# Kernel tuning notes

Hardware: AMD Instinct MI355X
Metric: run time of the kernel (lower is better)

Reference implementation:

```python
import jax, jax.numpy as jnp
import numpy as np

NUM_NODES = 113      # nodes (ROIs) per graph, from __init__ default
NUM_GRAPHS = 4096    # graphs in the batch
IN_DIM, HID, EMB = 3, 128, 1024
GROUPS = 8
EPS = 1e-5


def _kaiming(key, fan_in, fan_out_dim, shape):
    # kaiming_normal_(mode='fan_out', nonlinearity='leaky_relu') with default a=sqrt(5)->gain irrelevant here;
    # torch uses gain = sqrt(2/(1+0.01^2)) for leaky_relu default slope; simple faithful-scale normal init.
    gain = jnp.sqrt(2.0 / (1.0 + 0.01 ** 2)).astype(jnp.float32)
    std = gain / jnp.sqrt(jnp.float32(fan_out_dim))
    return jax.random.normal(key, shape, dtype=jnp.float32) * std


def setup_inputs() -> dict:
    key = jax.random.key(0)
    ks = jax.random.split(key, 8)
    N = NUM_GRAPHS * NUM_NODES
    x = jax.random.normal(ks[0], (N, IN_DIM), dtype=jnp.float32)
    batch = jnp.repeat(jnp.arange(NUM_GRAPHS, dtype=jnp.int32), NUM_NODES)
    return {
        "x": x,
        "roi_scaler": jnp.ones((NUM_NODES, IN_DIM), dtype=jnp.float32),
        "W1": _kaiming(ks[1], IN_DIM, HID, (IN_DIM, HID)),
        "b1": jnp.zeros((HID,), jnp.float32),
        "gn_g": jnp.ones((HID,), jnp.float32),
        "gn_b": jnp.zeros((HID,), jnp.float32),
        "W2": _kaiming(ks[2], HID, HID, (HID, HID)),
        "b2": jnp.zeros((HID,), jnp.float32),
        "W3": _kaiming(ks[3], HID, 512, (HID, 512)),
        "b3": jnp.zeros((512,), jnp.float32),
        "bn_g": jnp.ones((512,), jnp.float32),
        "bn_b": jnp.zeros((512,), jnp.float32),
        "W4": _kaiming(ks[4], 512, EMB, (512, EMB)),
        "b4": jnp.zeros((EMB,), jnp.float32),
        "batch": batch,
    }


def _group_norm(h, gamma, beta):
    # torch GroupNorm on [N, C]: per-row, per-group normalization
    N, C = h.shape
    hg = h.reshape(N, GROUPS, C // GROUPS)
    mu = hg.mean(axis=-1, keepdims=True)
    var = hg.var(axis=-1, keepdims=True)
    hn = ((hg - mu) * jax.lax.rsqrt(var + EPS)).reshape(N, C)
    return hn * gamma + beta


def reference(x, roi_scaler, W1, b1, gn_g, gn_b, W2, b2, W3, b3, bn_g, bn_b, W4, b4, batch):
    # per-ROI learned scaling, tiled across graphs (node order is graph-major)
    h = x * jnp.tile(roi_scaler, (NUM_GRAPHS, 1))            # [N, 3]
    # node_net: Linear -> GroupNorm(8) -> LeakyReLU(0.2) -> Linear
    h = h @ W1 + b1                                          # [N, 128]
    h = _group_norm(h, gn_g, gn_b)
    h = jnp.where(h > 0, h, 0.2 * h)
    h = h @ W2 + b2                                          # [N, 128]
    # global_max_pool: segment max over graph id
    z = jax.ops.segment_max(h, batch, num_segments=NUM_GRAPHS)  # [G, 128]
    # projection: Linear -> BatchNorm1d (batch stats, no running stats) -> ReLU -> Linear
    p = z @ W3 + b3                                          # [G, 512]
    mu = p.mean(axis=0)
    var = p.var(axis=0)
    p = (p - mu) * jax.lax.rsqrt(var + EPS) * bn_g + bn_b
    p = jax.nn.relu(p)
    out = p @ W4 + b4                                        # [G, 1024]
    # F.normalize(p=2, dim=1)
    nrm = jnp.sqrt(jnp.sum(out * out, axis=1, keepdims=True))
    return out / jnp.maximum(nrm, 1e-12)
```

## Files before the change

kernel.cpp:

```cpp
#include <hip/hip_runtime.h>
#include <hip/hip_bf16.h>

typedef _Float16 f16_8 __attribute__((ext_vector_type(8)));
typedef _Float16 f16_4 __attribute__((ext_vector_type(4)));
typedef float f32x4 __attribute__((ext_vector_type(4)));

#define NNODES 113
#define NGRAPH 4096

#define Z_OFF    0u
#define PH_OFF   2097152u
#define PSUM_OFF 6291456u
#define PSQ_OFF  6815744u
#define PSN_OFF  7340032u
#define GC_OFF   10485760u
#define SA_OFF   10489856u
#define SD_OFF   10491904u
#define W2P_OFF  10493952u
#define W4P_OFF  10559488u

__global__ __launch_bounds__(256) void k0_prep(
    const float* __restrict__ W2, const float* __restrict__ W4,
    const float* __restrict__ W1, const float* __restrict__ b1,
    _Float16* __restrict__ w2p, _Float16* __restrict__ w4p,
    float* __restrict__ gc) {
  int b = blockIdx.x, t = threadIdx.x;
  if (b < 256) {
    __shared__ _Float16 T[32 * 72];
    int kt = b >> 4, nc = b & 15;
    int row = t >> 3, c8 = (t & 7) * 8;
    const float* src = &W4[(kt * 32 + row) * 1024 + nc * 64 + c8];
    float4 a0 = *(const float4*)src;
    float4 a1 = *(const float4*)(src + 4);
    f16_8 v = {(_Float16)a0.x, (_Float16)a0.y, (_Float16)a0.z, (_Float16)a0.w,
               (_Float16)a1.x, (_Float16)a1.y, (_Float16)a1.z, (_Float16)a1.w};
    *(f16_8*)&T[row * 72 + c8] = v;
    __syncthreads();
    int ntl = t >> 6, L = t & 63;
    f16_8 w;
#pragma unroll
    for (int j = 0; j < 8; j++)
      w[j] = T[((L >> 4) * 8 + j) * 72 + ntl * 16 + (L & 15)];
    *(f16_8*)&w4p[((kt * 64 + nc * 4 + ntl) * 64 + L) * 8] = w;
  } else if (b < 264) {
    int q0 = (b - 256) * 256 + t;
    int L = q0 & 63, nt = (q0 >> 6) & 7, kt = q0 >> 9;
    f16_8 v;
#pragma unroll
    for (int j = 0; j < 8; j++)
      v[j] = (_Float16)W2[(kt * 32 + ((L >> 4) << 3) + j) * 128 + (nt << 4) + (L & 15)];
    *(f16_8*)&w2p[((kt * 8 + nt) * 64 + L) * 8] = v;
  } else {
    if (t < 128) {
      float a0 = W1[t], a1 = W1[128 + t], a2 = W1[256 + t], bb = b1[t];
      float p[14] = {a0, a1, a2, bb,
                     a0 * a0, 2.f * a0 * a1, 2.f * a0 * a2,
                     a1 * a1, 2.f * a1 * a2, a2 * a2,
                     2.f * bb * a0, 2.f * bb * a1, 2.f * bb * a2, bb * bb};
#pragma unroll
      for (int m = 1; m < 16; m <<= 1)
#pragma unroll
        for (int k = 0; k < 14; k++) p[k] += __shfl_xor(p[k], m, 64);
      if ((t & 15) == 0) {
        int gg = t >> 4;
#pragma unroll
        for (int k = 0; k < 4; k++) gc[gg * 16 + k] = p[k] * 0.0625f;
#pragma unroll
        for (int k = 4; k < 14; k++) gc[gg * 16 + k] = p[k];
      }
    }
  }
}

__global__ __launch_bounds__(256, 4) void k1_nodenet(
    const float* __restrict__ x, const float* __restrict__ roi,
    const float* __restrict__ W1, const float* __restrict__ b1,
    const float* __restrict__ gn_g, const float* __restrict__ gn_b,
    const _Float16* __restrict__ w2p, const float* __restrict__ b2,
    const float* __restrict__ gc, float* __restrict__ z) {
  __shared__ float4 xs4[NNODES];
  __shared__ _Float16 A[128 * 136];
  int t = threadIdx.x, g = blockIdx.x;
  int lane = t & 63, wv = t >> 6, quad = lane >> 4, l16 = lane & 15;

  int o = t & 15;
  int gq = o >> 1;
  float gcv[14];
#pragma unroll
  for (int j = 0; j < 14; j++) gcv[j] = gc[gq * 16 + j];

  float pw0[8], pw1[8], pw2[8], pb[8], pg[8], pbe[8];
#pragma unroll
  for (int j = 0; j < 8; j++) {
    int c = o * 8 + j;
    pw0[j] = W1[c]; pw1[j] = W1[128 + c]; pw2[j] = W1[256 + c];
    pb[j] = b1[c];  pg[j] = gn_g[c];      pbe[j] = gn_b[c];
  }

  f16_8 bh[4][2];
#pragma unroll
  for (int kt = 0; kt < 4; kt++)
#pragma unroll
    for (int ni = 0; ni < 2; ni++)
      bh[kt][ni] = *(const f16_8*)&w2p[((kt * 8 + wv * 2 + ni) * 64 + lane) * 8];

  for (int i = t; i < NNODES * 3; i += 256) {
    float v = x[g * (NNODES * 3) + i] * roi[i];
    ((float*)xs4)[(i / 3) * 4 + (i % 3)] = v;
  }
  __syncthreads();

  for (int it = t; it < 2048; it += 256) {
    int n = it >> 4;
    f16_8 hv;
    if (n < NNODES) {
      float4 xv = xs4[n];
      float mu = fmaf(xv.z, gcv[2], fmaf(xv.y, gcv[1], fmaf(xv.x, gcv[0], gcv[3])));
      float qf = fmaf(xv.z, gcv[12], fmaf(xv.y, gcv[11], fmaf(xv.x, gcv[10], gcv[13])));
      float u0 = fmaf(xv.z, gcv[6], fmaf(xv.y, gcv[5], xv.x * gcv[4]));
      qf = fmaf(xv.x, u0, qf);
      float u1 = fmaf(xv.z, gcv[8], xv.y * gcv[7]);
      qf = fmaf(xv.y, u1, qf);
      qf = fmaf(xv.z * xv.z, gcv[9], qf);
      float var = fmaxf(qf * 0.0625f - mu * mu, 0.0f);
      float ia = rsqrtf(var + 1e-5f);
      float ib = -mu * ia;
#pragma unroll
      for (int j = 0; j < 8; j++) {
        float h = fmaf(xv.z, pw2[j], fmaf(xv.y, pw1[j], fmaf(xv.x, pw0[j], pb[j])));
        float y = fmaf(fmaf(h, ia, ib), pg[j], pbe[j]);
        y = (y > 0.0f) ? y : 0.2f * y;
        hv[j] = (_Float16)y;
      }
    } else {
#pragma unroll
      for (int j = 0; j < 8; j++) hv[j] = (_Float16)0.f;
    }
    *(f16_8*)&A[n * 136 + o * 8] = hv;
  }
  __syncthreads();

  f32x4 acc[2][8];
#pragma unroll
  for (int a = 0; a < 2; a++)
#pragma unroll
    for (int m = 0; m < 8; m++) acc[a][m] = (f32x4){0.f, 0.f, 0.f, 0.f};

#pragma unroll
  for (int kt = 0; kt < 4; kt++) {
    f16_8 ah[8];
#pragma unroll
    for (int mt = 0; mt < 8; mt++)
      ah[mt] = *(const f16_8*)&A[(mt * 16 + l16) * 136 + kt * 32 + quad * 8];
#pragma unroll
    for (int ni = 0; ni < 2; ni++)
#pragma unroll
      for (int mt = 0; mt < 8; mt++)
        acc[ni][mt] = __builtin_amdgcn_mfma_f32_16x16x32_f16(ah[mt], bh[kt][ni], acc[ni][mt], 0, 0, 0);
  }

#pragma unroll
  for (int ni = 0; ni < 2; ni++) {
    int nt = wv * 2 + ni;
    float m = -3.4e38f;
#pragma unroll
    for (int mt = 0; mt < 8; mt++)
#pragma unroll
      for (int r = 0; r < 4; r++) {
        int row = mt * 16 + quad * 4 + r;
        if (row < NNODES) m = fmaxf(m, acc[ni][mt][r]);
      }
    m = fmaxf(m, __shfl_xor(m, 16, 64));
    m = fmaxf(m, __shfl_xor(m, 32, 64));
    if (quad == 0) {
      int col = nt * 16 + l16;
      z[g * 128 + col] = m + b2[col];
    }
  }
}

__global__ __launch_bounds__(256) void k2_proj(
    const float* __restrict__ z, const float* __restrict__ W3,
    const float* __restrict__ b3, _Float16* __restrict__ ph,
    float* __restrict__ psum, float* __restrict__ psq) {
  __shared__ float zs[16 * 128];
  __shared__ float reds[8 * 128];
  __shared__ float redq[8 * 128];
  int t = threadIdx.x;
  int rb = blockIdx.x >> 2, cbb = blockIdx.x & 3;
  int gr0 = rb * 16, cc0 = cbb * 128;
  for (int i = t; i < 2048; i += 256) zs[i] = z[gr0 * 128 + i];
  int cg = t & 31, rg = t >> 5;
  int cc = cc0 + cg * 4;
  float4 bb = *(const float4*)&b3[cc];
  float a0[4] = {0.f, 0.f, 0.f, 0.f}, a1[4] = {0.f, 0.f, 0.f, 0.f};
  __syncthreads();

#pragma unroll 8
  for (int k = 0; k < 128; k++) {
    float4 w = *(const float4*)&W3[k * 512 + cc];
    float z0 = zs[rg * 256 + k];
    float z1 = zs[rg * 256 + 128 + k];
    a0[0] = fmaf(z0, w.x, a0[0]); a0[1] = fmaf(z0, w.y, a0[1]);
    a0[2] = fmaf(z0, w.z, a0[2]); a0[3] = fmaf(z0, w.w, a0[3]);
    a1[0] = fmaf(z1, w.x, a1[0]); a1[1] = fmaf(z1, w.y, a1[1]);
    a1[2] = fmaf(z1, w.z, a1[2]); a1[3] = fmaf(z1, w.w, a1[3]);
  }
  int r0 = gr0 + rg * 2;
  f16_4 h0, h1;
  float s[4], q[4];
#pragma unroll
  for (int j = 0; j < 4; j++) {
    float v0 = a0[j] + ((float*)&bb)[j];
    float v1 = a1[j] + ((float*)&bb)[j];
    h0[j] = (_Float16)v0; h1[j] = (_Float16)v1;
    s[j] = v0 + v1;
    q[j] = fmaf(v0, v0, v1 * v1);
  }
  *(f16_4*)&ph[r0 * 512 + cc] = h0;
  *(f16_4*)&ph[(r0 + 1) * 512 + cc] = h1;
#pragma unroll
  for (int j = 0; j < 4; j++) {
    reds[rg * 128 + cg * 4 + j] = s[j];
    redq[rg * 128 + cg * 4 + j] = q[j];
  }
  __syncthreads();
  if (t < 128) {
    float ss = 0.f, qq = 0.f;
#pragma unroll
    for (int r = 0; r < 8; r++) { ss += reds[r * 128 + t]; qq += redq[r * 128 + t]; }
    psum[rb * 512 + cc0 + t] = ss;
    psq[rb * 512 + cc0 + t] = qq;
  }
}

__global__ __launch_bounds__(512) void k3_stats(
    const float* __restrict__ psum, const float* __restrict__ psq,
    const float* __restrict__ bn_g, const float* __restrict__ bn_b,
    float* __restrict__ sa, float* __restrict__ sd) {
  int c = threadIdx.x;
  float s = 0.f, q = 0.f;
#pragma unroll 8
  for (int b = 0; b < 256; b++) {
    s += psum[b * 512 + c];
    q += psq[b * 512 + c];
  }
  float mu = s * (1.0f / 4096.0f);
  float var = fmaxf(q * (1.0f / 4096.0f) - mu * mu, 0.0f);
  float sc = bn_g[c] * rsqrtf(var + 1e-5f);
  sa[c] = sc;
  sd[c] = bn_b[c] - mu * sc;
}

__global__ __launch_bounds__(256) void k4a_gemm(
    const _Float16* __restrict__ ph, const float* __restrict__ sa,
    const float* __restrict__ sd, const _Float16* __restrict__ w4p,
    const float* __restrict__ b4, float* __restrict__ out,
    float* __restrict__ psn) {
  __shared__ _Float16 T[2][64 * 40];
  __shared__ float sas[512], sds[512];
  __shared__ float rred[4 * 64];
  int t = threadIdx.x;
  int rb = blockIdx.x & 63, cb = blockIdx.x >> 6;
  int lane = t & 63, wv = t >> 6, quad = lane >> 4, l16 = lane & 15;

  for (int i = t; i < 512; i += 256) { sas[i] = sa[i]; sds[i] = sd[i]; }

  int srow = t >> 2, seg8 = (t & 3) * 8;
  const _Float16* prow = &ph[(rb * 64 + srow) * 512];
  f16_8 pa = *(const f16_8*)&prow[seg8];
  f16_8 bfr[2];
#pragma unroll
  for (int ni = 0; ni < 2; ni++)
    bfr[ni] = *(const f16_8*)&w4p[((cb * 8 + wv * 2 + ni) * 64 + lane) * 8];
  __syncthreads();

  {
    f16_8 v;
#pragma unroll
    for (int j = 0; j < 8; j++) {
      float vv = fmaf((float)pa[j], sas[seg8 + j], sds[seg8 + j]);
      v[j] = (_Float16)fmaxf(vv, 0.0f);
    }
    *(f16_8*)&T[0][srow * 40 + seg8] = v;
  }
  __syncthreads();

  f32x4 acc[2][4];
#pragma unroll
  for (int a = 0; a < 2; a++)
#pragma unroll
    for (int m = 0; m < 4; m++) acc[a][m] = (f32x4){0.f, 0.f, 0.f, 0.f};

  for (int kt = 0; kt < 16; kt++) {
    int nb = kt + 1;
    f16_8 na;
    if (nb < 16) na = *(const f16_8*)&prow[nb * 32 + seg8];
    f16_8 bc0 = bfr[0], bc1 = bfr[1];
    if (nb < 16) {
#pragma unroll
      for (int ni = 0; ni < 2; ni++)
        bfr[ni] = *(const f16_8*)&w4p[((nb * 64 + cb * 8 + wv * 2 + ni) * 64 + lane) * 8];
    }
    const _Float16* Tb = &T[kt & 1][0];
#pragma unroll
    for (int mt = 0; mt < 4; mt++) {
      f16_8 af = *(const f16_8*)&Tb[(mt * 16 + l16) * 40 + quad * 8];
      acc[0][mt] = __builtin_amdgcn_mfma_f32_16x16x32_f16(af, bc0, acc[0][mt], 0, 0, 0);
      acc[1][mt] = __builtin_amdgcn_mfma_f32_16x16x32_f16(af, bc1, acc[1][mt], 0, 0, 0);
    }
    if (nb < 16) {
      int kc = nb * 32 + seg8;
      f16_8 v;
#pragma unroll
      for (int j = 0; j < 8; j++) {
        float vv = fmaf((float)na[j], sas[kc + j], sds[kc + j]);
        v[j] = (_Float16)fmaxf(vv, 0.0f);
      }
      *(f16_8*)&T[nb & 1][srow * 40 + seg8] = v;
    }
    __syncthreads();
  }

  float rsq[4][4];
#pragma unroll
  for (int mt = 0; mt < 4; mt++)
#pragma unroll
    for (int r = 0; r < 4; r++) rsq[mt][r] = 0.0f;
#pragma unroll
  for (int ni = 0; ni < 2; ni++) {
    int col = cb * 128 + (wv * 2 + ni) * 16 + l16;
    float bv = b4[col];
#pragma unroll
    for (int mt = 0; mt < 4; mt++)
#pragma unroll
      for (int r = 0; r < 4; r++) {
        float v = acc[ni][mt][r] + bv;
        out[(rb * 64 + mt * 16 + quad * 4 + r) * 1024 + col] = v;
        rsq[mt][r] = fmaf(v, v, rsq[mt][r]);
      }
  }
#pragma unroll
  for (int m = 1; m < 16; m <<= 1)
#pragma unroll
    for (int mt = 0; mt < 4; mt++)
#pragma unroll
      for (int r = 0; r < 4; r++) rsq[mt][r] += __shfl_xor(rsq[mt][r], m, 64);
  if (l16 == 0) {
#pragma unroll
    for (int mt = 0; mt < 4; mt++)
#pragma unroll
      for (int r = 0; r < 4; r++)
        rred[wv * 64 + mt * 16 + quad * 4 + r] = rsq[mt][r];
  }
  __syncthreads();
  if (t < 64) {
    float s = rred[t] + rred[64 + t] + rred[128 + t] + rred[192 + t];
    psn[cb * 4096 + rb * 64 + t] = s;
  }
}

__global__ __launch_bounds__(256) void k4b_norm(
    float* __restrict__ out, const float* __restrict__ psn) {
  int t = threadIdx.x;
  int row = blockIdx.x * 4 + (t >> 6);
  float s = 0.f;
#pragma unroll
  for (int cb = 0; cb < 8; cb++) s += psn[cb * 4096 + row];
  float inv = 1.0f / fmaxf(sqrtf(s), 1e-12f);
  int c0 = (t & 63) * 4;
#pragma unroll
  for (int it = 0; it < 4; it++) {
    float4 v = *(const float4*)&out[row * 1024 + it * 256 + c0];
    v.x *= inv; v.y *= inv; v.z *= inv; v.w *= inv;
    *(float4*)&out[row * 1024 + it * 256 + c0] = v;
  }
}

extern "C" void kernel_launch(void* const* d_in, const int* in_sizes, int n_in,
                              void* d_out, int out_size, void* d_ws, size_t ws_size,
                              hipStream_t stream) {
  const float* x   = (const float*)d_in[0];
  const float* roi = (const float*)d_in[1];
  const float* W1  = (const float*)d_in[2];
  const float* b1  = (const float*)d_in[3];
  const float* gng = (const float*)d_in[4];
  const float* gnb = (const float*)d_in[5];
  const float* W2  = (const float*)d_in[6];
  const float* b2  = (const float*)d_in[7];
  const float* W3  = (const float*)d_in[8];
  const float* b3  = (const float*)d_in[9];
  const float* bng = (const float*)d_in[10];
  const float* bnb = (const float*)d_in[11];
  const float* W4  = (const float*)d_in[12];
  const float* b4  = (const float*)d_in[13];
  float* out = (float*)d_out;

  char* ws = (char*)d_ws;
  float*    z    = (float*)(ws + Z_OFF);
  _Float16* ph   = (_Float16*)(ws + PH_OFF);
  float*    psum = (float*)(ws + PSUM_OFF);
  float*    psq  = (float*)(ws + PSQ_OFF);
  float*    psn  = (float*)(ws + PSN_OFF);
  float*    gc   = (float*)(ws + GC_OFF);
  float*    sa   = (float*)(ws + SA_OFF);
  float*    sd   = (float*)(ws + SD_OFF);
  _Float16* w2p  = (_Float16*)(ws + W2P_OFF);
  _Float16* w4p  = (_Float16*)(ws + W4P_OFF);

  k0_prep<<<265, 256, 0, stream>>>(W2, W4, W1, b1, w2p, w4p, gc);
  k1_nodenet<<<NGRAPH, 256, 0, stream>>>(x, roi, W1, b1, gng, gnb, w2p, b2, gc, z);
  k2_proj<<<1024, 256, 0, stream>>>(z, W3, b3, ph, psum, psq);
  k3_stats<<<1, 512, 0, stream>>>(psum, psq, bng, bnb, sa, sd);
  k4a_gemm<<<512, 256, 0, stream>>>(ph, sa, sd, w4p, b4, out, psn);
  k4b_norm<<<1024, 256, 0, stream>>>(out, psn);
}
```

Baseline: 175.7 us.

## Fuse BN stats and L2 normalize into producer kernels via last-block atomic counters

Removes the separate single-block BN-stats kernel and the row-normalize kernel. The last block of k2_proj, found through an atomic counter, computes the BatchNorm scale and shift. In k4a_gemm, the last of the 8 column blocks for each row block rescales the 64 output rows. This saves two kernel launches and their gaps, but puts serial tail work on single blocks and adds fences and atomics to every block. The counters are zeroed in the prep kernel on each call.

Measured after the change: 343.5 us. 95.5% more time.

```diff
diff --git a/kernel.cpp b/kernel.cpp
--- a/kernel.cpp
+++ b/kernel.cpp
@@ -14,6 +14,7 @@
 #define PSQ_OFF  6815744u
 #define PSN_OFF  7340032u
 #define GC_OFF   10485760u
+#define CNT_OFF  10486272u
 #define SA_OFF   10489856u
 #define SD_OFF   10491904u
 #define W2P_OFF  10493952u
@@ -23,7 +24,7 @@
     const float* __restrict__ W2, const float* __restrict__ W4,
     const float* __restrict__ W1, const float* __restrict__ b1,
     _Float16* __restrict__ w2p, _Float16* __restrict__ w4p,
-    float* __restrict__ gc) {
+    float* __restrict__ gc, int* __restrict__ cnt) {
   int b = blockIdx.x, t = threadIdx.x;
   if (b < 256) {
     __shared__ _Float16 T[32 * 72];
@@ -51,6 +52,7 @@
       v[j] = (_Float16)W2[(kt * 32 + ((L >> 4) << 3) + j) * 128 + (nt << 4) + (L & 15)];
     *(f16_8*)&w2p[((kt * 8 + nt) * 64 + L) * 8] = v;
   } else {
+    if (t >= 128 && t < 193) cnt[t - 128] = 0;
     if (t < 128) {
       float a0 = W1[t], a1 = W1[128 + t], a2 = W1[256 + t], bb = b1[t];
       float p[14] = {a0, a1, a2, bb,
@@ -182,10 +184,13 @@
 __global__ __launch_bounds__(256) void k2_proj(
     const float* __restrict__ z, const float* __restrict__ W3,
     const float* __restrict__ b3, _Float16* __restrict__ ph,
-    float* __restrict__ psum, float* __restrict__ psq) {
+    float* __restrict__ psum, float* __restrict__ psq,
+    const float* __restrict__ bn_g, const float* __restrict__ bn_b,
+    float* __restrict__ sa, float* __restrict__ sd, int* __restrict__ cnt) {
   __shared__ float zs[16 * 128];
   __shared__ float reds[8 * 128];
   __shared__ float redq[8 * 128];
+  __shared__ int lastFlag;
   int t = threadIdx.x;
   int rb = blockIdx.x >> 2, cbb = blockIdx.x & 3;
   int gr0 = rb * 16, cc0 = cbb * 128;
@@ -232,34 +237,38 @@
     psum[rb * 512 + cc0 + t] = ss;
     psq[rb * 512 + cc0 + t] = qq;
   }
-}
-
-__global__ __launch_bounds__(512) void k3_stats(
-    const float* __restrict__ psum, const float* __restrict__ psq,
-    const float* __restrict__ bn_g, const float* __restrict__ bn_b,
-    float* __restrict__ sa, float* __restrict__ sd) {
-  int c = threadIdx.x;
-  float s = 0.f, q = 0.f;
+  __threadfence();
+  __syncthreads();
+  if (t == 0) lastFlag = (atomicAdd(&cnt[0], 1) == 1023);
+  __syncthreads();
+  if (lastFlag) {
+    __threadfence();
+    for (int c = t; c < 512; c += 256) {
+      float ss = 0.f, qq = 0.f;
 #pragma unroll 8
-  for (int b = 0; b < 256; b++) {
-    s += psum[b * 512 + c];
-    q += psq[b * 512 + c];
-  }
-  float mu = s * (1.0f / 4096.0f);
-  float var = fmaxf(q * (1.0f / 4096.0f) - mu * mu, 0.0f);
-  float sc = bn_g[c] * rsqrtf(var + 1e-5f);
-  sa[c] = sc;
-  sd[c] = bn_b[c] - mu * sc;
+      for (int b = 0; b < 256; b++) {
+        ss += psum[b * 512 + c];
+        qq += psq[b * 512 + c];
+      }
+      float mu = ss * (1.0f / 4096.0f);
+      float var = fmaxf(qq * (1.0f / 4096.0f) - mu * mu, 0.0f);
+      float sc = bn_g[c] * rsqrtf(var + 1e-5f);
+      sa[c] = sc;
+      sd[c] = bn_b[c] - mu * sc;
+    }
+  }
 }
 
 __global__ __launch_bounds__(256) void k4a_gemm(
     const _Float16* __restrict__ ph, const float* __restrict__ sa,
     const float* __restrict__ sd, const _Float16* __restrict__ w4p,
     const float* __restrict__ b4, float* __restrict__ out,
-    float* __restrict__ psn) {
+    float* __restrict__ psn, int* __restrict__ cnt4) {
   __shared__ _Float16 T[2][64 * 40];
   __shared__ float sas[512], sds[512];
   __shared__ float rred[4 * 64];
+  __shared__ float sinv[64];
+  __shared__ int lastFlag;
   int t = threadIdx.x;
   int rb = blockIdx.x & 63, cb = blockIdx.x >> 6;
   int lane = t & 63, wv = t >> 6, quad = lane >> 4, l16 = lane & 15;
@@ -358,22 +367,28 @@
     float s = rred[t] + rred[64 + t] + rred[128 + t] + rred[192 + t];
     psn[cb * 4096 + rb * 64 + t] = s;
   }
-}
-
-__global__ __launch_bounds__(256) void k4b_norm(
-    float* __restrict__ out, const float* __restrict__ psn) {
-  int t = threadIdx.x;
-  int row = blockIdx.x * 4 + (t >> 6);
-  float s = 0.f;
-#pragma unroll
-  for (int cb = 0; cb < 8; cb++) s += psn[cb * 4096 + row];
-  float inv = 1.0f / fmaxf(sqrtf(s), 1e-12f);
-  int c0 = (t & 63) * 4;
-#pragma unroll
-  for (int it = 0; it < 4; it++) {
-    float4 v = *(const float4*)&out[row * 1024 + it * 256 + c0];
-    v.x *= inv; v.y *= inv; v.z *= inv; v.w *= inv;
-    *(float4*)&out[row * 1024 + it * 256 + c0] = v;
+  __threadfence();
+  __syncthreads();
+  if (t == 0) lastFlag = (atomicAdd(&cnt4[rb], 1) == 7);
+  __syncthreads();
+  if (lastFlag) {
+    __threadfence();
+    if (t < 64) {
+      int row = rb * 64 + t;
+      float s = 0.f;
+#pragma unroll
+      for (int c = 0; c < 8; c++) s += psn[c * 4096 + row];
+      sinv[t] = 1.0f / fmaxf(sqrtf(s), 1e-12f);
+    }
+    __syncthreads();
+#pragma unroll 4
+    for (int i = t; i < 64 * 256; i += 256) {
+      int row = i >> 8, c4 = (i & 255) * 4;
+      float iv = sinv[row];
+      float4 v = *(const float4*)&out[(rb * 64 + row) * 1024 + c4];
+      v.x *= iv; v.y *= iv; v.z *= iv; v.w *= iv;
+      *(float4*)&out[(rb * 64 + row) * 1024 + c4] = v;
+    }
   }
 }
 
@@ -403,15 +418,14 @@
   float*    psq  = (float*)(ws + PSQ_OFF);
   float*    psn  = (float*)(ws + PSN_OFF);
   float*    gc   = (float*)(ws + GC_OFF);
+  int*      cnt  = (int*)(ws + CNT_OFF);
   float*    sa   = (float*)(ws + SA_OFF);
   float*    sd   = (float*)(ws + SD_OFF);
   _Float16* w2p  = (_Float16*)(ws + W2P_OFF);
   _Float16* w4p  = (_Float16*)(ws + W4P_OFF);
 
-  k0_prep<<<265, 256, 0, stream>>>(W2, W4, W1, b1, w2p, w4p, gc);
+  k0_prep<<<265, 256, 0, stream>>>(W2, W4, W1, b1, w2p, w4p, gc, cnt);
   k1_nodenet<<<NGRAPH, 256, 0, stream>>>(x, roi, W1, b1, gng, gnb, w2p, b2, gc, z);
-  k2_proj<<<1024, 256, 0, stream>>>(z, W3, b3, ph, psum, psq);
-  k3_stats<<<1, 512, 0, stream>>>(psum, psq, bng, bnb, sa, sd);
-  k4a_gemm<<<512, 256, 0, stream>>>(ph, sa, sd, w4p, b4, out, psn);
-  k4b_norm<<<1024, 256, 0, stream>>>(out, psn);
+  k2_proj<<<1024, 256, 0, stream>>>(z, W3, b3, ph, psum, psq, bng, bnb, sa, sd, cnt);
+  k4a_gemm<<<512, 256, 0, stream>>>(ph, sa, sd, w4p, b4, out, psn, cnt + 1);
 }
```
